# Kernel tuning notes

Measured on AMD Instinct MI355X. Metric: run time of the kernel, lower is better.

The kernel has to match this reference:

```python
import jax, jax.numpy as jnp
import numpy as np


def setup_inputs() -> dict:
    key = jax.random.key(0)
    k1, k2, k3 = jax.random.split(key, 3)
    B, Cin, H, W = 16, 128, 56, 56
    Cout, Kh, Kw = 256, 3, 3
    tensor = jax.random.normal(k1, (B, Cin, H, W), dtype=jnp.float32)
    weights = jax.random.normal(k2, (Cout, Cin, Kh, Kw), dtype=jnp.float32) * 0.05
    bias = jax.random.normal(k3, (Cout,), dtype=jnp.float32) * 0.05
    return {"tensor": tensor, "weights": weights, "bias": bias}


def reference(tensor, weights, bias):
    # OpticalConvolution: unfold (im2col) -> per-output-channel augmented dot
    # products (w . patch + b). Mathematically this is a standard 2D conv with
    # bias, expressed here as one fused conv instead of a per-channel loop.
    stride, padding, dilation = (1, 1), ((1, 1), (1, 1)), (1, 1)
    out = jax.lax.conv_general_dilated(
        tensor, weights,
        window_strides=stride,
        padding=padding,
        rhs_dilation=dilation,
        dimension_numbers=("NCHW", "OIHW", "NCHW"),
    )
    return out + bias[None, :, None, None]  # [B, Cout, H_out, W_out]
```

## Files before the change

kernel.cpp:

```cpp
#include <hip/hip_runtime.h>
#include <hip/hip_bf16.h>

typedef unsigned short ushort_t;
typedef unsigned int uint_t;

#define CIN   128
#define COUT  256
#define HH    56
#define WW    56
#define HWSZ  3136
#define BATCH 16
#define NPIX  50176
#define KTOT  1152

#define PROW_U 68
#define PATCH_U (4 * 58 * 68)

typedef __attribute__((ext_vector_type(8))) short bf16x8;
typedef __attribute__((ext_vector_type(4))) float f32x4;

__device__ __forceinline__ ushort_t f2bf(float v) {
    union { float f; uint_t u; } c; c.f = v;
    uint_t u = c.u;
    u += 0x7FFFu + ((u >> 16) & 1u);
    return (ushort_t)(u >> 16);
}

__device__ __forceinline__ uint_t pk2bf(float lo, float hi) {
    __hip_bfloat162 h = __float22bfloat162_rn(make_float2(lo, hi));
    union { __hip_bfloat162 h; uint_t u; } c; c.h = h;
    return c.u;
}

__global__ __launch_bounds__(256) void wprep(
    const float* __restrict__ weights, ushort_t* __restrict__ A2)
{
    __shared__ ushort_t lds_s[KTOT];
    const int tid = threadIdx.x;
    const int co  = blockIdx.x;
    const float* src = weights + (size_t)co * KTOT;
    #pragma unroll
    for (int k = 0; k < 5; ++k) {
        int idx = tid + k * 256;
        if (idx < KTOT) {
            int ci  = idx / 9;
            int pos = idx - ci * 9;
            lds_s[pos * 128 + ci] = f2bf(src[idx]);
        }
    }
    __syncthreads();
    int mt  = co >> 6;
    int ii  = (co >> 4) & 3;
    int l16 = co & 15;
    if (tid < 144) {
        int s    = tid >> 2;
        int quad = tid & 3;
        uint4 v = *(const uint4*)&lds_s[(s >> 2) * 128 + (s & 3) * 32 + quad * 8];
        *(uint4*)(A2 + ((size_t)((mt * 36 + s) * 4 + ii) * 64 + quad * 16 + l16) * 8) = v;
    }
}

__global__ __launch_bounds__(256, 2) void conv_direct(
    const ushort_t* __restrict__ A2,
    const float* __restrict__ tensor,
    const float* __restrict__ bias,
    float* __restrict__ out)
{
    __shared__ __align__(16) uint_t patch[PATCH_U];
    const int tid  = threadIdx.x;
    const int wave = tid >> 6;
    const int lane = tid & 63;
    const int quad = lane >> 4;
    const int l16  = lane & 15;

    const int bn = blockIdx.x;
    const int b  = bn / 28;
    const int y0 = (bn - b * 28) * 2;

    #pragma unroll
    for (int k = 0; k < 16; ++k) {
        int i4 = tid + k * 256;
        if (i4 < PATCH_U / 4) *(uint4*)&patch[i4 * 4] = make_uint4(0u, 0u, 0u, 0u);
    }
    __syncthreads();

    const float* src_b = tensor + (size_t)b * CIN * HWSZ;
    #pragma unroll
    for (int it = 0; it < 16; ++it) {
        int xq = tid & 15;
        int t2 = it * 16 + (tid >> 4);
        int cp = t2 & 63;
        int pr = t2 >> 6;
        int y  = y0 - 1 + pr;
        if (xq < 14 && (uint_t)y < (uint_t)HH) {
            const float* s0 = src_b + (size_t)(2 * cp) * HWSZ + y * WW + xq * 4;
            float4 va = *(const float4*)s0;
            float4 vb = *(const float4*)(s0 + HWSZ);
            uint_t* dst = &patch[(pr * 58 + xq * 4 + 1) * PROW_U + cp];
            dst[0 * PROW_U] = pk2bf(va.x, vb.x);
            dst[1 * PROW_U] = pk2bf(va.y, vb.y);
            dst[2 * PROW_U] = pk2bf(va.z, vb.z);
            dst[3 * PROW_U] = pk2bf(va.w, vb.w);
        }
    }
    __syncthreads();

    const ushort_t* patch_s = (const ushort_t*)patch;
    int bbase[7];
    #pragma unroll
    for (int j = 0; j < 7; ++j) {
        int p  = j * 16 + l16;
        int ro = p / 56;
        int x  = p - ro * 56;
        bbase[j] = (ro * 58 + x) * 136 + quad * 8;
    }

    const ushort_t* aPtr = A2 + ((size_t)(wave * 144) * 64 + lane) * 8;
    bf16x8 aCur[4], aNxt[4];
    #pragma unroll
    for (int i = 0; i < 4; ++i) aCur[i] = *(const bf16x8*)(aPtr + i * 512);

    const f32x4 zero = {0.f, 0.f, 0.f, 0.f};
    f32x4 acc[4][7];
    #pragma unroll
    for (int i = 0; i < 4; ++i)
        #pragma unroll
        for (int j = 0; j < 7; ++j) acc[i][j] = zero;

    #pragma unroll
    for (int pos = 0; pos < 9; ++pos) {
        const int dy = pos / 3 - 1;
        const int dx = pos % 3 - 1;
        const int poff = ((dy + 1) * 58 + (dx + 1)) * 136;
        #pragma unroll
        for (int cc = 0; cc < 4; ++cc) {
            const int s = pos * 4 + cc;
            if (s < 35) {
                aPtr += 2048;
                #pragma unroll
                for (int i = 0; i < 4; ++i)
                    aNxt[i] = *(const bf16x8*)(aPtr + i * 512);
            }
            bf16x8 bfr[7];
            #pragma unroll
            for (int j = 0; j < 7; ++j)
                bfr[j] = *(const bf16x8*)&patch_s[bbase[j] + poff + cc * 32];
            #pragma unroll
            for (int i = 0; i < 4; ++i)
                #pragma unroll
                for (int j = 0; j < 7; ++j)
                    acc[i][j] = __builtin_amdgcn_mfma_f32_16x16x32_bf16(
                        aCur[i], bfr[j], acc[i][j], 0, 0, 0);
            #pragma unroll
            for (int i = 0; i < 4; ++i) aCur[i] = aNxt[i];
        }
    }

    int opix[7];
    #pragma unroll
    for (int j = 0; j < 7; ++j) {
        int p  = j * 16 + l16;
        int ro = p / 56;
        int x  = p - ro * 56;
        opix[j] = (y0 + ro) * WW + x;
    }
    const size_t bout = (size_t)b * (COUT * HWSZ);
    #pragma unroll
    for (int i = 0; i < 4; ++i) {
        #pragma unroll
        for (int r = 0; r < 4; ++r) {
            int co = wave * 64 + i * 16 + quad * 4 + r;
            float bv = bias[co];
            size_t obase = bout + (size_t)co * HWSZ;
            #pragma unroll
            for (int j = 0; j < 7; ++j)
                out[obase + opix[j]] = acc[i][j][r] + bv;
        }
    }
}

__global__ void naive_conv(const float* __restrict__ in, const float* __restrict__ w,
                           const float* __restrict__ bias, float* __restrict__ out, int total) {
    int idx = blockIdx.x * 256 + threadIdx.x;
    if (idx >= total) return;
    int x = idx % WW; int t = idx / WW;
    int y = t % HH; t /= HH;
    int co = t % COUT; int b = t / COUT;
    float s = bias[co];
    const float* wr = w + (size_t)co * KTOT;
    for (int ci = 0; ci < CIN; ++ci) {
        const float* ir = in + (size_t)(b * CIN + ci) * HWSZ;
        for (int kh = 0; kh < 3; ++kh) {
            int yy = y + kh - 1;
            if ((uint_t)yy >= (uint_t)HH) continue;
            for (int kw = 0; kw < 3; ++kw) {
                int xx = x + kw - 1;
                if ((uint_t)xx >= (uint_t)WW) continue;
                s += ir[yy * WW + xx] * wr[ci * 9 + kh * 3 + kw];
            }
        }
    }
    out[idx] = s;
}

extern "C" void kernel_launch(void* const* d_in, const int* in_sizes, int n_in,
                              void* d_out, int out_size, void* d_ws, size_t ws_size,
                              hipStream_t stream) {
    const float* tensor  = (const float*)d_in[0];
    const float* weights = (const float*)d_in[1];
    const float* bias    = (const float*)d_in[2];
    float* out = (float*)d_out;

    const size_t A2_BYTES = (size_t)COUT * KTOT * 2;

    if (ws_size >= A2_BYTES) {
        ushort_t* A2 = (ushort_t*)d_ws;
        wprep<<<COUT, 256, 0, stream>>>(weights, A2);
        conv_direct<<<NPIX / 112, 256, 0, stream>>>(A2, tensor, bias, out);
    } else {
        int total = BATCH * COUT * HWSZ;
        naive_conv<<<(total + 255) / 256, 256, 0, stream>>>(tensor, weights, bias, out, total);
    }
}
```

Measured before the change: 110.3 us.

## Zero only halo cells in LDS patch and double-buffer B fragments

Replaces the full LDS patch clear and its barrier with zeroing of just the border columns, plus top or bottom rows at image edges. The main loop is flattened into 36 steps and now prefetches the next step's B fragments from LDS together with the A fragments from global memory. The goal is to overlap LDS read latency with MFMA work and cut redundant stores and a sync. It costs extra vector registers, which may reduce occupancy.

```diff
diff --git a/kernel.cpp b/kernel.cpp
--- a/kernel.cpp
+++ b/kernel.cpp
@@ -77,12 +77,24 @@
     const int b  = bn / 28;
     const int y0 = (bn - b * 28) * 2;
 
-    #pragma unroll
-    for (int k = 0; k < 16; ++k) {
-        int i4 = tid + k * 256;
-        if (i4 < PATCH_U / 4) *(uint4*)&patch[i4 * 4] = make_uint4(0u, 0u, 0u, 0u);
-    }
-    __syncthreads();
+    const uint4 z4 = make_uint4(0u, 0u, 0u, 0u);
+    for (int t = tid; t < 204; t += 256) {
+        int cell = t / 17, part = t - cell * 17;
+        int pr = cell >> 1, xc = (cell & 1) * 57;
+        *(uint4*)&patch[(pr * 58 + xc) * PROW_U + part * 4] = z4;
+    }
+    if (y0 == 0) {
+        for (int t = tid; t < 986; t += 256) {
+            int cell = t / 17, part = t - cell * 17;
+            *(uint4*)&patch[cell * PROW_U + part * 4] = z4;
+        }
+    }
+    if (y0 == 54) {
+        for (int t = tid; t < 986; t += 256) {
+            int cell = t / 17, part = t - cell * 17;
+            *(uint4*)&patch[(3 * 58 + cell) * PROW_U + part * 4] = z4;
+        }
+    }
 
     const float* src_b = tensor + (size_t)b * CIN * HWSZ;
     #pragma unroll
@@ -106,19 +118,16 @@
     __syncthreads();
 
     const ushort_t* patch_s = (const ushort_t*)patch;
-    int bbase[7];
+    const ushort_t* bptr[7];
     #pragma unroll
     for (int j = 0; j < 7; ++j) {
         int p  = j * 16 + l16;
         int ro = p / 56;
         int x  = p - ro * 56;
-        bbase[j] = (ro * 58 + x) * 136 + quad * 8;
-    }
-
-    const ushort_t* aPtr = A2 + ((size_t)(wave * 144) * 64 + lane) * 8;
-    bf16x8 aCur[4], aNxt[4];
-    #pragma unroll
-    for (int i = 0; i < 4; ++i) aCur[i] = *(const bf16x8*)(aPtr + i * 512);
+        bptr[j] = patch_s + (ro * 58 + x) * 136 + quad * 8;
+    }
+
+    const ushort_t* aBase = A2 + ((size_t)(wave * 144) * 64 + lane) * 8;
 
     const f32x4 zero = {0.f, 0.f, 0.f, 0.f};
     f32x4 acc[4][7];
@@ -127,33 +136,36 @@
         #pragma unroll
         for (int j = 0; j < 7; ++j) acc[i][j] = zero;
 
-    #pragma unroll
-    for (int pos = 0; pos < 9; ++pos) {
-        const int dy = pos / 3 - 1;
-        const int dx = pos % 3 - 1;
-        const int poff = ((dy + 1) * 58 + (dx + 1)) * 136;
-        #pragma unroll
-        for (int cc = 0; cc < 4; ++cc) {
-            const int s = pos * 4 + cc;
-            if (s < 35) {
-                aPtr += 2048;
-                #pragma unroll
-                for (int i = 0; i < 4; ++i)
-                    aNxt[i] = *(const bf16x8*)(aPtr + i * 512);
-            }
-            bf16x8 bfr[7];
+    bf16x8 aCur[4], aNxt[4], bCur[7], bNxt[7];
+    #pragma unroll
+    for (int i = 0; i < 4; ++i) aCur[i] = *(const bf16x8*)(aBase + i * 512);
+    #pragma unroll
+    for (int j = 0; j < 7; ++j) bCur[j] = *(const bf16x8*)(bptr[j]);
+
+    #pragma unroll
+    for (int s = 0; s < 36; ++s) {
+        if (s < 35) {
+            const int s1   = s + 1;
+            const int pos1 = s1 >> 2;
+            const int cc1  = s1 & 3;
+            const int off1 = ((pos1 / 3) * 58 + (pos1 % 3)) * 136 + cc1 * 32;
+            #pragma unroll
+            for (int i = 0; i < 4; ++i)
+                aNxt[i] = *(const bf16x8*)(aBase + (size_t)(s1 * 4 + i) * 512);
             #pragma unroll
             for (int j = 0; j < 7; ++j)
-                bfr[j] = *(const bf16x8*)&patch_s[bbase[j] + poff + cc * 32];
-            #pragma unroll
-            for (int i = 0; i < 4; ++i)
-                #pragma unroll
-                for (int j = 0; j < 7; ++j)
-                    acc[i][j] = __builtin_amdgcn_mfma_f32_16x16x32_bf16(
-                        aCur[i], bfr[j], acc[i][j], 0, 0, 0);
-            #pragma unroll
-            for (int i = 0; i < 4; ++i) aCur[i] = aNxt[i];
-        }
+                bNxt[j] = *(const bf16x8*)(bptr[j] + off1);
+        }
+        #pragma unroll
+        for (int i = 0; i < 4; ++i)
+            #pragma unroll
+            for (int j = 0; j < 7; ++j)
+                acc[i][j] = __builtin_amdgcn_mfma_f32_16x16x32_bf16(
+                    aCur[i], bCur[j], acc[i][j], 0, 0, 0);
+        #pragma unroll
+        for (int i = 0; i < 4; ++i) aCur[i] = aNxt[i];
+        #pragma unroll
+        for (int j = 0; j < 7; ++j) bCur[j] = bNxt[j];
     }
 
     int opix[7];
```

New measurement: 111.2 us. Within noise of the previous version (+0.8%).
